# Kernel optimization log

Measured on AMD Instinct MI355X. Metric: run time of the kernel, lower is better.

## Reference

```python
import jax, jax.numpy as jnp
import numpy as np


def gcn_conv(x, W, b, src, dst, edge_weight):
    """GCNConv: out = A_hat @ (x @ W) + b, with A_hat given as an edge list.
    x: [N, F_in], W: [F_in, F_out], src/dst: [E] int, edge_weight: [E]."""
    N = x.shape[0]
    support = x @ W                                   # [N, F_out] dense GEMM
    msgs = support[src] * edge_weight[:, None]        # [E, F_out] gather + scale
    agg = jax.ops.segment_sum(msgs, dst, num_segments=N)  # [N, F_out] scatter-add
    return agg + b


def setup_inputs() -> dict:
    key = jax.random.key(0)
    ks = jax.random.split(key, 8)
    N, E, F_IN, H, D = 100000, 1600000, 256, 128, 64
    feature = jax.random.normal(ks[0], (N, F_IN), dtype=jnp.float32)
    src = jax.random.randint(ks[1], (E,), 0, N)
    dst = jax.random.randint(ks[2], (E,), 0, N)
    edge_weight = jax.random.uniform(ks[3], (E,), dtype=jnp.float32)
    W1 = jax.random.normal(ks[4], (F_IN, H), dtype=jnp.float32) / np.sqrt(F_IN).astype(np.float32)
    b1 = jnp.zeros((H,), jnp.float32)
    W2 = jax.random.normal(ks[5], (H, D), dtype=jnp.float32) / np.sqrt(H).astype(np.float32)
    b2 = jnp.zeros((D,), jnp.float32)
    return {"feature": feature, "src": src, "dst": dst, "edge_weight": edge_weight,
            "W1": W1, "b1": b1, "W2": W2, "b2": b2}


def reference(feature, src, dst, edge_weight, W1, b1, W2, b2):
    # layer 1: GCNConv -> relu (dropout is identity in eval mode)
    x1 = jax.nn.relu(gcn_conv(feature, W1, b1, src, dst, edge_weight))
    # layer 2: GCNConv -> log_softmax over feature dim
    x2 = gcn_conv(x1, W2, b2, src, dst, edge_weight)
    return (x1, jax.nn.log_softmax(x2, axis=1))
```

## Files before the change

kernel.cpp:

```cpp
#include <hip/hip_runtime.h>
#include <hip/hip_bf16.h>
#include <type_traits>


typedef unsigned short u16;
typedef unsigned char  u8;

__device__ __forceinline__ u16 f2bf(float x) {
    union { float f; unsigned u; } v; v.f = x;
    const unsigned r = v.u + 0x7FFFu + ((v.u >> 16) & 1u);
    return (u16)(r >> 16);
}
__device__ __forceinline__ float bf2f(unsigned h) {
    union { unsigned u; float f; } v; v.u = h << 16;
    return v.f;
}
__device__ __forceinline__ float uaf(unsigned u) {
    union { unsigned u; float f; } v; v.u = u;
    return v.f;
}
__device__ __forceinline__ unsigned fau(float f) {
    union { float f; unsigned u; } v; v.f = f;
    return v.u;
}

using short8  = __attribute__((ext_vector_type(8))) short;
using float4v = __attribute__((ext_vector_type(4))) float;

#define TILE_A 8192

template <typename AT, int BNt>
__device__ __forceinline__ void gemm_body(
    const int bix, const AT* __restrict__ A, const u16* __restrict__ BT,
    u16* __restrict__ C, const int M, const int K)
{
    constexpr int BMt = 128;
    constexpr int WAVES_N = BNt / 64;
    constexpr int WROWS = 4 / WAVES_N;
    constexpr int WMF = BMt / (16 * WROWS);
    constexpr int WNF = 4;

    __shared__ __align__(16) u16 As[BMt * 32];
    __shared__ __align__(16) u16 Bs[BNt * 32];

    const int tid  = threadIdx.x;
    const int lane = tid & 63;
    const int w    = tid >> 6;
    const int m0   = bix * BMt;

    const int wm = (w % WROWS) * (WMF * 16);
    const int wn = (w / WROWS) * 64;

    const int fm = lane & 15;
    const int kh = lane >> 4;

    float4v acc[WMF][WNF] = {};

    for (int k0 = 0; k0 < K; k0 += 32) {
        __syncthreads();
        if constexpr (std::is_same<AT, float>::value) {
#pragma unroll
            for (int i = 0; i < 4; ++i) {
                const int s   = i * 256 + tid;
                const int row = s >> 3;
                const int seg = s & 7;
                const int gr  = min(m0 + row, M - 1);
                const float4 v = *(const float4*)&A[(size_t)gr * K + k0 + seg * 4];
                ushort4 o;
                o.x = f2bf(v.x); o.y = f2bf(v.y); o.z = f2bf(v.z); o.w = f2bf(v.w);
                *(ushort4*)&As[row * 32 + seg * 4] = o;
            }
        } else {
#pragma unroll
            for (int i = 0; i < 2; ++i) {
                const int s   = i * 256 + tid;
                const int row = s >> 2;
                const int seg = s & 3;
                const int gr  = min(m0 + row, M - 1);
                *(uint4*)&As[row * 32 + seg * 8] =
                    *(const uint4*)&A[(size_t)gr * K + k0 + seg * 8];
            }
        }
#pragma unroll
        for (int i = 0; i < BNt * 4 / 256; ++i) {
            const int s   = i * 256 + tid;
            const int row = s >> 2;
            const int seg = s & 3;
            *(uint4*)&Bs[row * 32 + seg * 8] =
                *(const uint4*)&BT[(size_t)row * K + k0 + seg * 8];
        }
        __syncthreads();

        short8 af[WMF], bfr[WNF];
#pragma unroll
        for (int i = 0; i < WMF; ++i)
            af[i] = *(const short8*)&As[(wm + i * 16 + fm) * 32 + kh * 8];
#pragma unroll
        for (int j = 0; j < WNF; ++j)
            bfr[j] = *(const short8*)&Bs[(wn + j * 16 + fm) * 32 + kh * 8];
#pragma unroll
        for (int i = 0; i < WMF; ++i)
#pragma unroll
            for (int j = 0; j < WNF; ++j)
                acc[i][j] = __builtin_amdgcn_mfma_f32_16x16x32_bf16(
                    af[i], bfr[j], acc[i][j], 0, 0, 0);
    }

#pragma unroll
    for (int i = 0; i < WMF; ++i) {
#pragma unroll
        for (int j = 0; j < WNF; ++j) {
            const int col = wn + j * 16 + fm;
#pragma unroll
            for (int r = 0; r < 4; ++r) {
                const int row = m0 + wm + i * 16 + kh * 4 + r;
                if (row < M) C[(size_t)row * BNt + col] = f2bf(acc[i][j][r]);
            }
        }
    }
}

__global__ __launch_bounds__(256) void gemm2_k(
    const float* __restrict__ A, const u16* __restrict__ BT,
    u16* __restrict__ C, int M, int K)
{
    gemm_body<float, 64>(blockIdx.x, A, BT, C, M, K);
}

__global__ __launch_bounds__(256) void sortA1_k(
    const int* __restrict__ dst, int* __restrict__ G, int E, int NBLK, int NB,
    const float* __restrict__ W1, u16* __restrict__ W1T, int K1, int N1,
    const float* __restrict__ W2, u16* __restrict__ W2T, int K2, int N2)
{
    const int b = blockIdx.x;
    if (b >= NBLK) {
        const int t = (b - NBLK) * 256 + threadIdx.x;
        const int tot1 = K1 * N1;
        if (t < tot1) {
            const int k = t % K1, nn = t / K1;
            W1T[(size_t)nn * K1 + k] = f2bf(W1[(size_t)k * N1 + nn]);
        } else {
            const int t2 = t - tot1;
            if (t2 < K2 * N2) {
                const int k = t2 % K2, nn = t2 / K2;
                W2T[(size_t)nn * K2 + k] = f2bf(W2[(size_t)k * N2 + nn]);
            }
        }
        return;
    }

    __shared__ int hist[512];
    for (int i = threadIdx.x; i < NB; i += 256) hist[i] = 0;
    __syncthreads();
    const int base = b * TILE_A;
#pragma unroll 4
    for (int i = 0; i < TILE_A; i += 256) {
        const int e = base + i + threadIdx.x;
        if (e < E) atomicAdd(&hist[((unsigned)dst[e]) >> 8], 1);
    }
    __syncthreads();
    for (int i = threadIdx.x; i < NB; i += 256)
        G[(size_t)i * NBLK + b] = hist[i];
}


#define SCAN_B 256
#define SCAN_I 8
#define SCAN_TILE (SCAN_B * SCAN_I)

__global__ __launch_bounds__(SCAN_B) void scan_pass1(
    const int* __restrict__ in, int* __restrict__ out,
    int* __restrict__ blockSums, int n)
{
    __shared__ int waveSums[SCAN_B / 64];
    const int tid = threadIdx.x;
    const int lane = tid & 63;
    const int wid = tid >> 6;
    const int base = blockIdx.x * SCAN_TILE + tid * SCAN_I;

    int items[SCAN_I];
    int tsum = 0;
#pragma unroll
    for (int i = 0; i < SCAN_I; ++i) {
        const int idx = base + i;
        items[i] = (idx < n) ? in[idx] : 0;
        tsum += items[i];
    }
    int x = tsum;
#pragma unroll
    for (int o = 1; o < 64; o <<= 1) {
        const int y = __shfl_up(x, o, 64);
        if (lane >= o) x += y;
    }
    if (lane == 63) waveSums[wid] = x;
    __syncthreads();
    if (tid == 0) {
        int acc = 0;
#pragma unroll
        for (int w = 0; w < SCAN_B / 64; ++w) {
            const int t = waveSums[w]; waveSums[w] = acc; acc += t;
        }
        blockSums[blockIdx.x] = acc;
    }
    __syncthreads();
    int texcl = x - tsum + waveSums[wid];
#pragma unroll
    for (int i = 0; i < SCAN_I; ++i) {
        const int idx = base + i;
        if (idx < n) out[idx] = texcl;
        texcl += items[i];
    }
}

__global__ void scan_pass2(int* __restrict__ blockSums, int nb)
{
    const int lane = threadIdx.x;
    int run = 0;
    for (int base = 0; base < nb; base += 64) {
        const int idx = base + lane;
        const int v = (idx < nb) ? blockSums[idx] : 0;
        int x = v;
#pragma unroll
        for (int o = 1; o < 64; o <<= 1) {
            const int y = __shfl_up(x, o, 64);
            if (lane >= o) x += y;
        }
        if (idx < nb) blockSums[idx] = run + x - v;
        run += __shfl(x, 63, 64);
    }
}

__global__ __launch_bounds__(SCAN_B) void scan3G_k(
    int* __restrict__ G, const int* __restrict__ blockSums, int n,
    int* __restrict__ offs, int N, int E)
{
    const int idx = blockIdx.x * blockDim.x + threadIdx.x;
    if (idx < n) G[idx] += blockSums[idx / SCAN_TILE];
    if (idx == 0) offs[N] = E;
}

__global__ __launch_bounds__(256) void sortA2_k(
    const int* __restrict__ src, const int* __restrict__ dst,
    const float* __restrict__ ew, const int* __restrict__ G,
    uint2* __restrict__ eps, u8* __restrict__ ldst, int E, int NBLK, int NB)
{
    const int b = blockIdx.x;
    __shared__ int cur[512];
    for (int i = threadIdx.x; i < NB; i += 256)
        cur[i] = G[(size_t)i * NBLK + b];
    __syncthreads();
    const int base = b * TILE_A;
#pragma unroll 4
    for (int i = 0; i < TILE_A; i += 256) {
        const int e = base + i + threadIdx.x;
        if (e < E) {
            const int d = dst[e];
            const int p = atomicAdd(&cur[((unsigned)d) >> 8], 1);
            eps[p]  = make_uint2((unsigned)src[e], fau(ew[e]));
            ldst[p] = (u8)(d & 255);
        }
    }
}

__global__ __launch_bounds__(256) void megaB_k(
    const uint2* __restrict__ eps, const u8* __restrict__ ldst,
    const int* __restrict__ G, int* __restrict__ offs,
    uint2* __restrict__ epack, int E, int NBLK, int NB, int N,
    const float* __restrict__ A, const u16* __restrict__ BT,
    u16* __restrict__ C, int M, int K, int GB)
{
    const int b = blockIdx.x;
    const int third = b / 3;
    int sort_id = -1, gemm_id = -1;
    if ((b % 3) == 0 && third < NB) sort_id = third;
    else gemm_id = b - min((b + 2) / 3, NB);

    if (gemm_id >= 0) {
        if (gemm_id < GB) gemm_body<float, 128>(gemm_id, A, BT, C, M, K);
        return;
    }

    const int tid = threadIdx.x;
    const int sb = sort_id;
    const int start = G[(size_t)sb * NBLK];
    const int endv  = (sb + 1 < NB) ? G[(size_t)(sb + 1) * NBLK] : E;

    __shared__ int h[256];
    __shared__ int wsum[4];
    h[tid] = 0;
    __syncthreads();
    for (int i = start + tid; i < endv; i += 256)
        atomicAdd(&h[ldst[i]], 1);
    __syncthreads();

    const int lane = tid & 63;
    const int w = tid >> 6;
    const int v = h[tid];
    int x = v;
#pragma unroll
    for (int o = 1; o < 64; o <<= 1) {
        const int y = __shfl_up(x, o, 64);
        if (lane >= o) x += y;
    }
    if (lane == 63) wsum[w] = x;
    __syncthreads();
    if (tid == 0) {
        int a = 0;
#pragma unroll
        for (int q = 0; q < 4; ++q) { const int t = wsum[q]; wsum[q] = a; a += t; }
    }
    __syncthreads();
    const int excl = start + (x - v) + wsum[w];

    const int node = sb * 256 + tid;
    if (node < N) offs[node] = excl;

    __syncthreads();
    h[tid] = excl;
    __syncthreads();

    for (int i = start + tid; i < endv; i += 256) {
        const uint2 ep = eps[i];
        const int p = atomicAdd(&h[ldst[i]], 1);
        epack[p] = ep;
    }
}


__global__ __launch_bounds__(256) void agg_f128b(
    const u16* __restrict__ sup, const int* __restrict__ offs,
    const uint2* __restrict__ epack, const float* __restrict__ bias,
    float* __restrict__ out, int N)
{
    const int node = (blockIdx.x * blockDim.x + threadIdx.x) >> 4;
    const int hl = threadIdx.x & 15;
    if (node >= N) return;

    const int beg = offs[node];
    const int end = offs[node + 1];

    float a[2][8] = {};
    for (int j = beg; j < end; j += 8) {
        uint2 e[8];
#pragma unroll
        for (int i = 0; i < 8; ++i) {
            const int jj = (j + i < end) ? (j + i) : (end - 1);
            e[i] = epack[jj];
        }
#pragma unroll
        for (int i = 0; i < 8; ++i)
            if (j + i >= end) e[i].y = 0u;
        uint4 v[8];
#pragma unroll
        for (int i = 0; i < 8; ++i)
            v[i] = *(const uint4*)&sup[(size_t)e[i].x * 128 + hl * 8];
#pragma unroll
        for (int i = 0; i < 8; ++i) {
            const float w = uaf(e[i].y);
            float* acc = a[i & 1];
            acc[0] = fmaf(bf2f(v[i].x & 0xffffu), w, acc[0]);
            acc[1] = fmaf(bf2f(v[i].x >> 16),     w, acc[1]);
            acc[2] = fmaf(bf2f(v[i].y & 0xffffu), w, acc[2]);
            acc[3] = fmaf(bf2f(v[i].y >> 16),     w, acc[3]);
            acc[4] = fmaf(bf2f(v[i].z & 0xffffu), w, acc[4]);
            acc[5] = fmaf(bf2f(v[i].z >> 16),     w, acc[5]);
            acc[6] = fmaf(bf2f(v[i].w & 0xffffu), w, acc[6]);
            acc[7] = fmaf(bf2f(v[i].w >> 16),     w, acc[7]);
        }
    }
    const float4 b0 = *(const float4*)&bias[hl * 8];
    const float4 b1 = *(const float4*)&bias[hl * 8 + 4];
    float4v o0, o1;
    o0[0] = fmaxf(a[0][0] + a[1][0] + b0.x, 0.f);
    o0[1] = fmaxf(a[0][1] + a[1][1] + b0.y, 0.f);
    o0[2] = fmaxf(a[0][2] + a[1][2] + b0.z, 0.f);
    o0[3] = fmaxf(a[0][3] + a[1][3] + b0.w, 0.f);
    o1[0] = fmaxf(a[0][4] + a[1][4] + b1.x, 0.f);
    o1[1] = fmaxf(a[0][5] + a[1][5] + b1.y, 0.f);
    o1[2] = fmaxf(a[0][6] + a[1][6] + b1.z, 0.f);
    o1[3] = fmaxf(a[0][7] + a[1][7] + b1.w, 0.f);
    float4v* orow = (float4v*)&out[(size_t)node * 128 + hl * 8];
    orow[0] = o0;
    orow[1] = o1;
}

__global__ __launch_bounds__(256) void agg_f64_lsm(
    const u16* __restrict__ sup, const int* __restrict__ offs,
    const uint2* __restrict__ epack, const float* __restrict__ bias,
    float* __restrict__ out, int N)
{
    const int node = (blockIdx.x * blockDim.x + threadIdx.x) >> 4;
    const int hl = threadIdx.x & 15;
    if (node >= N) return;

    const int beg = offs[node];
    const int end = offs[node + 1];

    float a[2][4] = {};
    for (int j = beg; j < end; j += 8) {
        uint2 e[8];
#pragma unroll
        for (int i = 0; i < 8; ++i) {
            const int jj = (j + i < end) ? (j + i) : (end - 1);
            e[i] = epack[jj];
        }
#pragma unroll
        for (int i = 0; i < 8; ++i)
            if (j + i >= end) e[i].y = 0u;
        uint2 v[8];
#pragma unroll
        for (int i = 0; i < 8; ++i)
            v[i] = *(const uint2*)&sup[(size_t)e[i].x * 64 + hl * 4];
#pragma unroll
        for (int i = 0; i < 8; ++i) {
            const float w = uaf(e[i].y);
            float* acc = a[i & 1];
            acc[0] = fmaf(bf2f(v[i].x & 0xffffu), w, acc[0]);
            acc[1] = fmaf(bf2f(v[i].x >> 16),     w, acc[1]);
            acc[2] = fmaf(bf2f(v[i].y & 0xffffu), w, acc[2]);
            acc[3] = fmaf(bf2f(v[i].y >> 16),     w, acc[3]);
        }
    }

    const float4 b4 = *(const float4*)&bias[hl * 4];
    float z[4];
    z[0] = a[0][0] + a[1][0] + b4.x;
    z[1] = a[0][1] + a[1][1] + b4.y;
    z[2] = a[0][2] + a[1][2] + b4.z;
    z[3] = a[0][3] + a[1][3] + b4.w;

    float m = fmaxf(fmaxf(z[0], z[1]), fmaxf(z[2], z[3]));
#pragma unroll
    for (int o = 8; o > 0; o >>= 1) m = fmaxf(m, __shfl_xor(m, o, 64));
    float s = __expf(z[0] - m) + __expf(z[1] - m) + __expf(z[2] - m) + __expf(z[3] - m);
#pragma unroll
    for (int o = 8; o > 0; o >>= 1) s += __shfl_xor(s, o, 64);
    const float ls = __logf(s);
    *(float4*)&out[(size_t)node * 64 + hl * 4] =
        make_float4(z[0] - m - ls, z[1] - m - ls, z[2] - m - ls, z[3] - m - ls);
}


extern "C" void kernel_launch(void* const* d_in, const int* in_sizes, int n_in,
                              void* d_out, int out_size, void* d_ws, size_t ws_size,
                              hipStream_t stream) {
    const float* feature = (const float*)d_in[0];
    const int*   src     = (const int*)d_in[1];
    const int*   dst     = (const int*)d_in[2];
    const float* ew      = (const float*)d_in[3];
    const float* W1      = (const float*)d_in[4];
    const float* b1      = (const float*)d_in[5];
    const float* W2      = (const float*)d_in[6];
    const float* b2      = (const float*)d_in[7];

    const int E    = in_sizes[1];
    const int H    = in_sizes[5];
    const int D    = in_sizes[7];
    const int F_IN = in_sizes[4] / H;
    const int N    = in_sizes[0] / F_IN;

    float* out_x1 = (float*)d_out;
    float* out_x2 = (float*)d_out + (size_t)N * H;

    const int NB   = (N + 255) >> 8;
    const int NBLK = (E + TILE_A - 1) / TILE_A;
    const int nG   = NB * NBLK;
    const int GB   = (N + 127) / 128;

    char* ws = (char*)d_ws;
    auto carve = [&](size_t bytes) {
        char* p = ws;
        ws += (bytes + 15) & ~(size_t)15;
        return p;
    };
    int*   G         = (int*)  carve((size_t)nG * sizeof(int));
    int*   blockSums = (int*)  carve(4096 * sizeof(int));
    int*   offs      = (int*)  carve((size_t)(N + 1) * sizeof(int));
    uint2* epack     = (uint2*)carve((size_t)E * sizeof(uint2));
    u16*   W1T       = (u16*)  carve((size_t)H * F_IN * sizeof(u16));
    u16*   W2T       = (u16*)  carve((size_t)D * H * sizeof(u16));
    u16*   supbf     = (u16*)  carve((size_t)N * H * sizeof(u16));
    u16*   scratch   = (u16*)  carve((size_t)N * H * sizeof(u16));
    uint2* eps  = (uint2*)scratch;
    u8*    ldst = (u8*)scratch + (size_t)E * sizeof(uint2);

    {
        const int TCB = (F_IN * H + H * D + 255) / 256;
        sortA1_k<<<NBLK + TCB, 256, 0, stream>>>(
            dst, G, E, NBLK, NB, W1, W1T, F_IN, H, W2, W2T, H, D);
    }

    const int nScanBlocks = (nG + SCAN_TILE - 1) / SCAN_TILE;
    scan_pass1<<<nScanBlocks, SCAN_B, 0, stream>>>(G, G, blockSums, nG);
    scan_pass2<<<1, 64, 0, stream>>>(blockSums, nScanBlocks);
    scan3G_k<<<(nG + SCAN_B - 1) / SCAN_B, SCAN_B, 0, stream>>>(
        G, blockSums, nG, offs, N, E);

    sortA2_k<<<NBLK, 256, 0, stream>>>(src, dst, ew, G, eps, ldst, E, NBLK, NB);

    {
        int grid = NB + GB;
        if (grid < 3 * NB - 2) grid = 3 * NB - 2;
        megaB_k<<<grid, 256, 0, stream>>>(
            eps, ldst, G, offs, epack, E, NBLK, NB, N,
            feature, W1T, supbf, N, F_IN, GB);
    }

    agg_f128b<<<(N * 16 + 255) / 256, 256, 0, stream>>>(
        supbf, offs, epack, b1, out_x1, N);

    gemm2_k<<<(N + 127) / 128, 256, 0, stream>>>(out_x1, W2T, supbf, N, H);
    agg_f64_lsm<<<(N * 16 + 255) / 256, 256, 0, stream>>>(
        supbf, offs, epack, b2, out_x2, N);
}
```

Baseline: 395.5 us.

## Fuse layer-2 GEMM into layer-1 aggregation kernel via shared-memory row projection

```diff
diff --git a/kernel.cpp b/kernel.cpp
--- a/kernel.cpp
+++ b/kernel.cpp
@@ -118,13 +118,6 @@
             }
         }
     }
-}
-
-__global__ __launch_bounds__(256) void gemm2_k(
-    const float* __restrict__ A, const u16* __restrict__ BT,
-    u16* __restrict__ C, int M, int K)
-{
-    gemm_body<float, 64>(blockIdx.x, A, BT, C, M, K);
 }
 
 __global__ __launch_bounds__(256) void sortA1_k(
@@ -327,61 +320,112 @@
 }
 
 
-__global__ __launch_bounds__(256) void agg_f128b(
+__global__ __launch_bounds__(256) void agg_f128b_g2(
     const u16* __restrict__ sup, const int* __restrict__ offs,
     const uint2* __restrict__ epack, const float* __restrict__ bias,
-    float* __restrict__ out, int N)
-{
-    const int node = (blockIdx.x * blockDim.x + threadIdx.x) >> 4;
-    const int hl = threadIdx.x & 15;
-    if (node >= N) return;
-
-    const int beg = offs[node];
-    const int end = offs[node + 1];
-
-    float a[2][8] = {};
-    for (int j = beg; j < end; j += 8) {
-        uint2 e[8];
-#pragma unroll
-        for (int i = 0; i < 8; ++i) {
-            const int jj = (j + i < end) ? (j + i) : (end - 1);
-            e[i] = epack[jj];
-        }
-#pragma unroll
-        for (int i = 0; i < 8; ++i)
-            if (j + i >= end) e[i].y = 0u;
-        uint4 v[8];
-#pragma unroll
-        for (int i = 0; i < 8; ++i)
-            v[i] = *(const uint4*)&sup[(size_t)e[i].x * 128 + hl * 8];
-#pragma unroll
-        for (int i = 0; i < 8; ++i) {
-            const float w = uaf(e[i].y);
-            float* acc = a[i & 1];
-            acc[0] = fmaf(bf2f(v[i].x & 0xffffu), w, acc[0]);
-            acc[1] = fmaf(bf2f(v[i].x >> 16),     w, acc[1]);
-            acc[2] = fmaf(bf2f(v[i].y & 0xffffu), w, acc[2]);
-            acc[3] = fmaf(bf2f(v[i].y >> 16),     w, acc[3]);
-            acc[4] = fmaf(bf2f(v[i].z & 0xffffu), w, acc[4]);
-            acc[5] = fmaf(bf2f(v[i].z >> 16),     w, acc[5]);
-            acc[6] = fmaf(bf2f(v[i].w & 0xffffu), w, acc[6]);
-            acc[7] = fmaf(bf2f(v[i].w >> 16),     w, acc[7]);
-        }
-    }
-    const float4 b0 = *(const float4*)&bias[hl * 8];
-    const float4 b1 = *(const float4*)&bias[hl * 8 + 4];
-    float4v o0, o1;
-    o0[0] = fmaxf(a[0][0] + a[1][0] + b0.x, 0.f);
-    o0[1] = fmaxf(a[0][1] + a[1][1] + b0.y, 0.f);
-    o0[2] = fmaxf(a[0][2] + a[1][2] + b0.z, 0.f);
-    o0[3] = fmaxf(a[0][3] + a[1][3] + b0.w, 0.f);
-    o1[0] = fmaxf(a[0][4] + a[1][4] + b1.x, 0.f);
-    o1[1] = fmaxf(a[0][5] + a[1][5] + b1.y, 0.f);
-    o1[2] = fmaxf(a[0][6] + a[1][6] + b1.z, 0.f);
-    o1[3] = fmaxf(a[0][7] + a[1][7] + b1.w, 0.f);
-    float4v* orow = (float4v*)&out[(size_t)node * 128 + hl * 8];
-    orow[0] = o0;
-    orow[1] = o1;
+    const float* __restrict__ W2, float* __restrict__ out,
+    u16* __restrict__ sup2, int N)
+{
+    __shared__ float xrow[16][128];
+    __shared__ __align__(16) u16 w2s[128 * 68];
+
+    const int tid = threadIdx.x;
+
+    {
+        const int k  = tid >> 1;
+        const int d0 = (tid & 1) << 5;
+        const float* srcp = &W2[k * 64 + d0];
+        u16* dstp = &w2s[k * 68 + d0];
+#pragma unroll
+        for (int i = 0; i < 4; ++i) {
+            const float4 va = *(const float4*)&srcp[i * 8];
+            const float4 vb = *(const float4*)&srcp[i * 8 + 4];
+            ushort4 oa, ob;
+            oa.x = f2bf(va.x); oa.y = f2bf(va.y); oa.z = f2bf(va.z); oa.w = f2bf(va.w);
+            ob.x = f2bf(vb.x); ob.y = f2bf(vb.y); ob.z = f2bf(vb.z); ob.w = f2bf(vb.w);
+            *(ushort4*)&dstp[i * 8]     = oa;
+            *(ushort4*)&dstp[i * 8 + 4] = ob;
+        }
+    }
+    __syncthreads();
+
+    const int node = (blockIdx.x * blockDim.x + tid) >> 4;
+    const int hl   = tid & 15;
+    const int nl   = tid >> 4;
+
+    if (node < N) {
+        const int beg = offs[node];
+        const int end = offs[node + 1];
+
+        float a[2][8] = {};
+        for (int j = beg; j < end; j += 8) {
+            uint2 e[8];
+#pragma unroll
+            for (int i = 0; i < 8; ++i) {
+                const int jj = (j + i < end) ? (j + i) : (end - 1);
+                e[i] = epack[jj];
+            }
+#pragma unroll
+            for (int i = 0; i < 8; ++i)
+                if (j + i >= end) e[i].y = 0u;
+            uint4 v[8];
+#pragma unroll
+            for (int i = 0; i < 8; ++i)
+                v[i] = *(const uint4*)&sup[(size_t)e[i].x * 128 + hl * 8];
+#pragma unroll
+            for (int i = 0; i < 8; ++i) {
+                const float w = uaf(e[i].y);
+                float* acc = a[i & 1];
+                acc[0] = fmaf(bf2f(v[i].x & 0xffffu), w, acc[0]);
+                acc[1] = fmaf(bf2f(v[i].x >> 16),     w, acc[1]);
+                acc[2] = fmaf(bf2f(v[i].y & 0xffffu), w, acc[2]);
+                acc[3] = fmaf(bf2f(v[i].y >> 16),     w, acc[3]);
+                acc[4] = fmaf(bf2f(v[i].z & 0xffffu), w, acc[4]);
+                acc[5] = fmaf(bf2f(v[i].z >> 16),     w, acc[5]);
+                acc[6] = fmaf(bf2f(v[i].w & 0xffffu), w, acc[6]);
+                acc[7] = fmaf(bf2f(v[i].w >> 16),     w, acc[7]);
+            }
+        }
+        const float4 b0 = *(const float4*)&bias[hl * 8];
+        const float4 b1 = *(const float4*)&bias[hl * 8 + 4];
+        float4v o0, o1;
+        o0[0] = fmaxf(a[0][0] + a[1][0] + b0.x, 0.f);
+        o0[1] = fmaxf(a[0][1] + a[1][1] + b0.y, 0.f);
+        o0[2] = fmaxf(a[0][2] + a[1][2] + b0.z, 0.f);
+        o0[3] = fmaxf(a[0][3] + a[1][3] + b0.w, 0.f);
+        o1[0] = fmaxf(a[0][4] + a[1][4] + b1.x, 0.f);
+        o1[1] = fmaxf(a[0][5] + a[1][5] + b1.y, 0.f);
+        o1[2] = fmaxf(a[0][6] + a[1][6] + b1.z, 0.f);
+        o1[3] = fmaxf(a[0][7] + a[1][7] + b1.w, 0.f);
+        float4v* orow = (float4v*)&out[(size_t)node * 128 + hl * 8];
+        orow[0] = o0;
+        orow[1] = o1;
+        *(float4v*)&xrow[nl][hl * 8]     = o0;
+        *(float4v*)&xrow[nl][hl * 8 + 4] = o1;
+    }
+
+    __builtin_amdgcn_wave_barrier();
+
+    if (node < N) {
+        float acc2[4] = {0.f, 0.f, 0.f, 0.f};
+        for (int k0 = 0; k0 < 128; k0 += 8) {
+            const float4 xa = *(const float4*)&xrow[nl][k0];
+            const float4 xb = *(const float4*)&xrow[nl][k0 + 4];
+            const float xk[8] = {xa.x, xa.y, xa.z, xa.w, xb.x, xb.y, xb.z, xb.w};
+#pragma unroll
+            for (int kk = 0; kk < 8; ++kk) {
+                const uint2 wv = *(const uint2*)&w2s[(k0 + kk) * 68 + hl * 4];
+                acc2[0] = fmaf(xk[kk], bf2f(wv.x & 0xffffu), acc2[0]);
+                acc2[1] = fmaf(xk[kk], bf2f(wv.x >> 16),     acc2[1]);
+                acc2[2] = fmaf(xk[kk], bf2f(wv.y & 0xffffu), acc2[2]);
+                acc2[3] = fmaf(xk[kk], bf2f(wv.y >> 16),     acc2[3]);
+            }
+        }
+        uint2 p;
+        p.x = (unsigned)f2bf(acc2[0]) | ((unsigned)f2bf(acc2[1]) << 16);
+        p.y = (unsigned)f2bf(acc2[2]) | ((unsigned)f2bf(acc2[3]) << 16);
+        *(uint2*)&sup2[(size_t)node * 64 + hl * 4] = p;
+    }
 }
 
 __global__ __launch_bounds__(256) void agg_f64_lsm(
@@ -483,6 +527,7 @@
     u16*   scratch   = (u16*)  carve((size_t)N * H * sizeof(u16));
     uint2* eps  = (uint2*)scratch;
     u8*    ldst = (u8*)scratch + (size_t)E * sizeof(uint2);
+    u16*   sup2 = scratch;
 
     {
         const int TCB = (F_IN * H + H * D + 255) / 256;
@@ -506,10 +551,9 @@
             feature, W1T, supbf, N, F_IN, GB);
     }
 
-    agg_f128b<<<(N * 16 + 255) / 256, 256, 0, stream>>>(
-        supbf, offs, epack, b1, out_x1, N);
-
-    gemm2_k<<<(N + 127) / 128, 256, 0, stream>>>(out_x1, W2T, supbf, N, H);
+    agg_f128b_g2<<<(N * 16 + 255) / 256, 256, 0, stream>>>(
+        supbf, offs, epack, b1, W2, out_x1, sup2, N);
+
     agg_f64_lsm<<<(N * 16 + 255) / 256, 256, 0, stream>>>(
-        supbf, offs, epack, b2, out_x2, N);
-}
+        sup2, offs, epack, b2, out_x2, N);
+}
```

Measured after the change: 418.7 us. 5.9% more time.

## Bucket nodes by degree and process aggregation in degree-sorted order

Applied to the files above, without the earlier changes.

```diff
diff --git a/kernel.cpp b/kernel.cpp
--- a/kernel.cpp
+++ b/kernel.cpp
@@ -232,11 +232,12 @@
 
 __global__ __launch_bounds__(SCAN_B) void scan3G_k(
     int* __restrict__ G, const int* __restrict__ blockSums, int n,
-    int* __restrict__ offs, int N, int E)
+    int* __restrict__ offs, int N, int E, int* __restrict__ bhist)
 {
     const int idx = blockIdx.x * blockDim.x + threadIdx.x;
     if (idx < n) G[idx] += blockSums[idx / SCAN_TILE];
     if (idx == 0) offs[N] = E;
+    if (idx < 16) bhist[idx] = 0;
 }
 
 __global__ __launch_bounds__(256) void sortA2_k(
@@ -327,14 +328,68 @@
 }
 
 
+__global__ __launch_bounds__(256) void degA_k(
+    const int* __restrict__ offs, int* __restrict__ bhist, int N)
+{
+    __shared__ int h[16];
+    if (threadIdx.x < 16) h[threadIdx.x] = 0;
+    __syncthreads();
+    const int n = blockIdx.x * 256 + threadIdx.x;
+    if (n < N) {
+        const int deg = offs[n + 1] - offs[n];
+        atomicAdd(&h[min(deg >> 3, 15)], 1);
+    }
+    __syncthreads();
+    if (threadIdx.x < 16 && h[threadIdx.x] > 0)
+        atomicAdd(&bhist[threadIdx.x], h[threadIdx.x]);
+}
+
+__global__ void degB_k(const int* __restrict__ bhist, int* __restrict__ bcur)
+{
+    if (threadIdx.x == 0) {
+        int acc = 0;
+        for (int i = 0; i < 16; ++i) { const int v = bhist[i]; bcur[i] = acc; acc += v; }
+    }
+}
+
+__global__ __launch_bounds__(256) void degC_k(
+    const int* __restrict__ offs, int* __restrict__ bcur,
+    int* __restrict__ perm, int N)
+{
+    __shared__ int h[16];
+    __shared__ int base[16];
+    if (threadIdx.x < 16) h[threadIdx.x] = 0;
+    __syncthreads();
+    const int n = blockIdx.x * 256 + threadIdx.x;
+    int b = 0;
+    if (n < N) {
+        const int deg = offs[n + 1] - offs[n];
+        b = min(deg >> 3, 15);
+        atomicAdd(&h[b], 1);
+    }
+    __syncthreads();
+    if (threadIdx.x < 16)
+        base[threadIdx.x] = (h[threadIdx.x] > 0)
+            ? atomicAdd(&bcur[threadIdx.x], h[threadIdx.x]) : 0;
+    __syncthreads();
+    if (threadIdx.x < 16) h[threadIdx.x] = base[threadIdx.x];
+    __syncthreads();
+    if (n < N) {
+        const int pos = atomicAdd(&h[b], 1);
+        perm[pos] = n;
+    }
+}
+
+
 __global__ __launch_bounds__(256) void agg_f128b(
     const u16* __restrict__ sup, const int* __restrict__ offs,
     const uint2* __restrict__ epack, const float* __restrict__ bias,
-    float* __restrict__ out, int N)
-{
-    const int node = (blockIdx.x * blockDim.x + threadIdx.x) >> 4;
+    const int* __restrict__ perm, float* __restrict__ out, int N)
+{
+    const int node0 = (blockIdx.x * blockDim.x + threadIdx.x) >> 4;
     const int hl = threadIdx.x & 15;
-    if (node >= N) return;
+    if (node0 >= N) return;
+    const int node = perm[node0];
 
     const int beg = offs[node];
     const int end = offs[node + 1];
@@ -387,11 +442,12 @@
 __global__ __launch_bounds__(256) void agg_f64_lsm(
     const u16* __restrict__ sup, const int* __restrict__ offs,
     const uint2* __restrict__ epack, const float* __restrict__ bias,
-    float* __restrict__ out, int N)
-{
-    const int node = (blockIdx.x * blockDim.x + threadIdx.x) >> 4;
+    const int* __restrict__ perm, float* __restrict__ out, int N)
+{
+    const int node0 = (blockIdx.x * blockDim.x + threadIdx.x) >> 4;
     const int hl = threadIdx.x & 15;
-    if (node >= N) return;
+    if (node0 >= N) return;
+    const int node = perm[node0];
 
     const int beg = offs[node];
     const int end = offs[node + 1];
@@ -466,6 +522,7 @@
     const int NBLK = (E + TILE_A - 1) / TILE_A;
     const int nG   = NB * NBLK;
     const int GB   = (N + 127) / 128;
+    const int NBN  = (N + 255) / 256;
 
     char* ws = (char*)d_ws;
     auto carve = [&](size_t bytes) {
@@ -481,8 +538,12 @@
     u16*   W2T       = (u16*)  carve((size_t)D * H * sizeof(u16));
     u16*   supbf     = (u16*)  carve((size_t)N * H * sizeof(u16));
     u16*   scratch   = (u16*)  carve((size_t)N * H * sizeof(u16));
-    uint2* eps  = (uint2*)scratch;
-    u8*    ldst = (u8*)scratch + (size_t)E * sizeof(uint2);
+    int*   perm      = (int*)  carve((size_t)N * sizeof(int));
+    int*   bmeta     = (int*)  carve(64 * sizeof(int));
+    uint2* eps   = (uint2*)scratch;
+    u8*    ldst  = (u8*)scratch + (size_t)E * sizeof(uint2);
+    int*   bhist = bmeta;
+    int*   bcur  = bmeta + 16;
 
     {
         const int TCB = (F_IN * H + H * D + 255) / 256;
@@ -494,7 +555,7 @@
     scan_pass1<<<nScanBlocks, SCAN_B, 0, stream>>>(G, G, blockSums, nG);
     scan_pass2<<<1, 64, 0, stream>>>(blockSums, nScanBlocks);
     scan3G_k<<<(nG + SCAN_B - 1) / SCAN_B, SCAN_B, 0, stream>>>(
-        G, blockSums, nG, offs, N, E);
+        G, blockSums, nG, offs, N, E, bhist);
 
     sortA2_k<<<NBLK, 256, 0, stream>>>(src, dst, ew, G, eps, ldst, E, NBLK, NB);
 
@@ -506,10 +567,14 @@
             feature, W1T, supbf, N, F_IN, GB);
     }
 
+    degA_k<<<NBN, 256, 0, stream>>>(offs, bhist, N);
+    degB_k<<<1, 64, 0, stream>>>(bhist, bcur);
+    degC_k<<<NBN, 256, 0, stream>>>(offs, bcur, perm, N);
+
     agg_f128b<<<(N * 16 + 255) / 256, 256, 0, stream>>>(
-        supbf, offs, epack, b1, out_x1, N);
+        supbf, offs, epack, b1, perm, out_x1, N);
 
     gemm2_k<<<(N + 127) / 128, 256, 0, stream>>>(out_x1, W2T, supbf, N, H);
     agg_f64_lsm<<<(N * 16 + 255) / 256, 256, 0, stream>>>(
-        supbf, offs, epack, b2, out_x2, N);
-}
+        supbf, offs, epack, b2, perm, out_x2, N);
+}
```

Result: slower. 407.6 us (+3.1%).
